# Optimization experiments

Hardware: AMD Instinct MI355X
Metric: run time of the kernel (lower is better)

Reference implementation:

```python
import jax, jax.numpy as jnp
import numpy as np


def _gen_grid(flow):
    # flow: [N, 2, H, W] -> grid [N, H, W, 2] in normalized [-1,1] coords
    N, _, H, W = flow.shape
    step_y = 2.0 / H
    step_x = 2.0 / W
    gy = jnp.arange(H, dtype=flow.dtype) * step_y + (-1.0 + 0.5 * step_y)
    gx = jnp.arange(W, dtype=flow.dtype) * step_x + (-1.0 + 0.5 * step_x)
    fp = jnp.transpose(flow, (0, 2, 3, 1))  # [N,H,W,2]
    fx = gx[None, None, :] + fp[..., 0]
    fy = gy[None, :, None] + fp[..., 1]
    fx = jnp.remainder(fx + 1.0, 2.0) - 1.0  # wrap x
    return jnp.stack([fx, fy], axis=-1)


def _grid_sample_bilinear(img, grid):
    # img: [N,C,H,W]; grid: [N,H,W,2] normalized, align_corners=False, zero padding
    N, C, H, W = img.shape
    ihwc = jnp.transpose(img, (0, 2, 3, 1))  # [N,H,W,C]
    x = (grid[..., 0] + 1.0) * (W * 0.5) - 0.5
    y = (grid[..., 1] + 1.0) * (H * 0.5) - 0.5
    x0 = jnp.floor(x)
    y0 = jnp.floor(y)
    tx = x - x0
    ty = y - y0
    x0i = x0.astype(jnp.int32)
    y0i = y0.astype(jnp.int32)
    n = jnp.arange(N)[:, None, None]

    def gather(yi, xi):
        valid = (xi >= 0) & (xi < W) & (yi >= 0) & (yi < H)
        v = ihwc[n, jnp.clip(yi, 0, H - 1), jnp.clip(xi, 0, W - 1)]  # [N,H,W,C]
        return v * valid[..., None].astype(img.dtype)

    out = (gather(y0i, x0i) * ((1 - tx) * (1 - ty))[..., None]
           + gather(y0i, x0i + 1) * (tx * (1 - ty))[..., None]
           + gather(y0i + 1, x0i) * ((1 - tx) * ty)[..., None]
           + gather(y0i + 1, x0i + 1) * (tx * ty)[..., None])
    return jnp.transpose(out, (0, 3, 1, 2))  # [N,C,H,W]


def _compose(flow_prev, img_prev, flow_curr, img_curr):
    grid = _gen_grid(flow_curr)
    return (flow_curr + _grid_sample_bilinear(flow_prev, grid),
            img_curr + _grid_sample_bilinear(img_prev, grid))


def setup_inputs() -> dict:
    key = jax.random.key(0)
    k1, k2 = jax.random.split(key)
    B, L, C, H, W = 4, 32, 32, 128, 128
    flows = jax.random.normal(k1, (B, L, 2, H, W), dtype=jnp.float32) * 0.05
    images = jax.random.normal(k2, (B, L, C, H, W), dtype=jnp.float32)
    return {"flows": flows, "images": images}


def reference(flows, images):
    B, L, _, H, W = flows.shape
    C = images.shape[2]
    cf, ci = flows, images
    step = 1
    while step < L:  # static log2(L) iterations
        Lp = L - step
        pf = cf[:, :-step].reshape(B * Lp, 2, H, W)
        pi = ci[:, :-step].reshape(B * Lp, C, H, W)
        qf = cf[:, step:].reshape(B * Lp, 2, H, W)
        qi = ci[:, step:].reshape(B * Lp, C, H, W)
        nf, ni = _compose(pf, pi, qf, qi)
        cf = jnp.concatenate([cf[:, :step], nf.reshape(B, Lp, 2, H, W)], axis=1)
        ci = jnp.concatenate([ci[:, :step], ni.reshape(B, Lp, C, H, W)], axis=1)
        step *= 2
    return ci
```

## Files before the change

kernel.cpp:

```cpp
#include <hip/hip_runtime.h>


constexpr int B_ = 4, L_ = 32, C_ = 32, H_ = 128, W_ = 128;
constexpr int HW = H_ * W_;
constexpr size_t SLICE_I = (size_t)C_ * HW;
constexpr size_t SLICE_F = (size_t)2  * HW;

typedef unsigned short ush;

__device__ __forceinline__ float b2f(ush u) {
    union { unsigned int i; float f; } v; v.i = ((unsigned int)u) << 16; return v.f;
}
__device__ __forceinline__ ush f2b(float f) {
    union { float f; unsigned int i; } v; v.f = f;
    unsigned int r = v.i + 0x7FFFu + ((v.i >> 16) & 1u);
    return (ush)(r >> 16);
}

__device__ __forceinline__ int swz8(int bid, int chunk) {
    return (bid & 7) * chunk + (bid >> 3);
}

__global__ __launch_bounds__(256)
void prepass_img(const float* __restrict__ src, ush* __restrict__ P,
                 ush* __restrict__ S, float* __restrict__ outN)
{
    constexpr int NB = 32 * 512;
    const int bid = swz8(blockIdx.x, NB / 8);
    const int wc = bid & 3, h = (bid >> 2) & 127, l = bid >> 9;
    __shared__ float lds[32 * 33];
    const int t = threadIdx.x;
    {
        const int c = t >> 3, wq = t & 7;
        const size_t off = (size_t)l * SLICE_I + (size_t)c * HW + h * W_ + wc * 32 + wq * 4;
        const float4 v = *(const float4*)(src + off);
        if (l == 0)
            *(float4*)(outN + off) = v;
        float* s = &lds[c * 33 + wq * 4];
        s[0] = v.x; s[1] = v.y; s[2] = v.z; s[3] = v.w;
    }
    __syncthreads();
    {
        const int pix = t >> 3, cc = t & 7;
        ushort4 o;
        o.x = f2b(lds[(cc * 4 + 0) * 33 + pix]);
        o.y = f2b(lds[(cc * 4 + 1) * 33 + pix]);
        o.z = f2b(lds[(cc * 4 + 2) * 33 + pix]);
        o.w = f2b(lds[(cc * 4 + 3) * 33 + pix]);
        const size_t poff = ((size_t)l * HW + h * W_ + wc * 32 + pix) * C_ + cc * 4;
        if (l == 0) *(ushort4*)(S + poff) = o;
        else        *(ushort4*)(P + poff) = o;
    }
}

__global__ __launch_bounds__(256)
void prepass_flow(const float* __restrict__ src, float* __restrict__ F0,
                  float* __restrict__ SF)
{
    constexpr int NB = 32 * HW / 256;
    const int i = swz8(blockIdx.x, NB / 8) * 256 + threadIdx.x;
    const int l = i >> 14;
    const int p = i & (HW - 1);
    const float f0 = src[(size_t)l * SLICE_F + p];
    const float f1 = src[(size_t)l * SLICE_F + HW + p];
    float* dst = (l == 0) ? SF : F0;
    *(float2*)(dst + (size_t)l * SLICE_F + (size_t)p * 2) = make_float2(f0, f1);
}

template<int STEP>
__global__ __launch_bounds__(256)
void compose(const float* __restrict__ Fcur, const ush* __restrict__ Icur,
             float* __restrict__ Fpong, ush* __restrict__ Ipong,
             ush* __restrict__ S, float* __restrict__ SF,
             float* __restrict__ outN)
{
#pragma clang fp contract(off)
    constexpr int NB = (32 - STEP) * 512;
    const int bid = swz8(blockIdx.x, NB / 8);
    const int wc = bid & 3, h = (bid >> 2) & 127, l = STEP + (bid >> 9);
    const int t = threadIdx.x, pix = t >> 3, cc = t & 7;
    const int w = wc * 32 + pix;
    const int p = h * W_ + w;
    const size_t sI = (size_t)l * SLICE_I;
    const size_t sF = (size_t)l * SLICE_F;

    const float2 fc = *(const float2*)(Fcur + sF + (size_t)p * 2);

    const float step_x = 2.0f / (float)W_;
    const float step_y = 2.0f / (float)H_;
    const float gx = (float)w * step_x + (-1.0f + 0.5f * step_x);
    const float gy = (float)h * step_y + (-1.0f + 0.5f * step_y);
    float fx = gx + fc.x;
    const float fy = gy + fc.y;
    {
        const float tt = fx + 1.0f;
        float r = fmodf(tt, 2.0f);
        if (r < 0.0f) r += 2.0f;
        fx = r - 1.0f;
    }
    const float x = (fx + 1.0f) * ((float)W_ * 0.5f) - 0.5f;
    const float y = (fy + 1.0f) * ((float)H_ * 0.5f) - 0.5f;
    const float x0f = floorf(x), y0f = floorf(y);
    const float tx = x - x0f, ty = y - y0f;
    const int x0 = (int)x0f, y0 = (int)y0f, x1 = x0 + 1, y1 = y0 + 1;
    const float w00 = (1.0f - tx) * (1.0f - ty);
    const float w10 = tx * (1.0f - ty);
    const float w01 = (1.0f - tx) * ty;
    const float w11 = tx * ty;
    const bool vx0 = (x0 >= 0) & (x0 < W_), vx1 = (x1 >= 0) & (x1 < W_);
    const bool vy0 = (y0 >= 0) & (y0 < H_), vy1 = (y1 >= 0) & (y1 < H_);
    const bool v00 = vy0 & vx0, v10 = vy0 & vx1, v01 = vy1 & vx0, v11 = vy1 & vx1;
    const int xc0 = x0 < 0 ? 0 : (x0 >= W_ ? W_ - 1 : x0);
    const int xc1 = x1 < 0 ? 0 : (x1 >= W_ ? W_ - 1 : x1);
    const int yc0 = y0 < 0 ? 0 : (y0 >= H_ ? H_ - 1 : y0);
    const int yc1 = y1 < 0 ? 0 : (y1 >= H_ ? H_ - 1 : y1);
    const int q00 = yc0 * W_ + xc0, q10 = yc0 * W_ + xc1;
    const int q01 = yc1 * W_ + xc0, q11 = yc1 * W_ + xc1;

    const int prev = l - STEP;
    const ush*   pI = (prev < STEP) ? (S  + (size_t)prev * SLICE_I)
                                    : (Icur + (size_t)prev * SLICE_I);
    const float* pF = (prev < STEP) ? (SF + (size_t)prev * SLICE_F)
                                    : (Fcur + (size_t)prev * SLICE_F);

    const ushort4 G00 = *(const ushort4*)(pI + (size_t)q00 * C_ + cc * 4);
    const ushort4 G10 = *(const ushort4*)(pI + (size_t)q10 * C_ + cc * 4);
    const ushort4 G01 = *(const ushort4*)(pI + (size_t)q01 * C_ + cc * 4);
    const ushort4 G11 = *(const ushort4*)(pI + (size_t)q11 * C_ + cc * 4);
    float4 g00 = make_float4(b2f(G00.x), b2f(G00.y), b2f(G00.z), b2f(G00.w));
    float4 g10 = make_float4(b2f(G10.x), b2f(G10.y), b2f(G10.z), b2f(G10.w));
    float4 g01 = make_float4(b2f(G01.x), b2f(G01.y), b2f(G01.z), b2f(G01.w));
    float4 g11 = make_float4(b2f(G11.x), b2f(G11.y), b2f(G11.z), b2f(G11.w));
    g00.x = v00 ? g00.x : 0.0f; g00.y = v00 ? g00.y : 0.0f;
    g00.z = v00 ? g00.z : 0.0f; g00.w = v00 ? g00.w : 0.0f;
    g10.x = v10 ? g10.x : 0.0f; g10.y = v10 ? g10.y : 0.0f;
    g10.z = v10 ? g10.z : 0.0f; g10.w = v10 ? g10.w : 0.0f;
    g01.x = v01 ? g01.x : 0.0f; g01.y = v01 ? g01.y : 0.0f;
    g01.z = v01 ? g01.z : 0.0f; g01.w = v01 ? g01.w : 0.0f;
    g11.x = v11 ? g11.x : 0.0f; g11.y = v11 ? g11.y : 0.0f;
    g11.z = v11 ? g11.z : 0.0f; g11.w = v11 ? g11.w : 0.0f;

    float4 samp;
    samp.x = ((g00.x * w00 + g10.x * w10) + g01.x * w01) + g11.x * w11;
    samp.y = ((g00.y * w00 + g10.y * w10) + g01.y * w01) + g11.y * w11;
    samp.z = ((g00.z * w00 + g10.z * w10) + g01.z * w01) + g11.z * w11;
    samp.w = ((g00.w * w00 + g10.w * w10) + g01.w * w01) + g11.w * w11;

    const ushort4 CU = *(const ushort4*)(Icur + sI + (size_t)p * C_ + cc * 4);
    float4 o;
    o.x = b2f(CU.x) + samp.x; o.y = b2f(CU.y) + samp.y;
    o.z = b2f(CU.z) + samp.z; o.w = b2f(CU.w) + samp.w;

    float2 fo;
    const bool doFlow = (cc == 0) && (STEP < 16);
    if (doFlow) {
        float2 A00 = *(const float2*)(pF + (size_t)q00 * 2);
        float2 A10 = *(const float2*)(pF + (size_t)q10 * 2);
        float2 A01 = *(const float2*)(pF + (size_t)q01 * 2);
        float2 A11 = *(const float2*)(pF + (size_t)q11 * 2);
        A00.x = v00 ? A00.x : 0.0f; A00.y = v00 ? A00.y : 0.0f;
        A10.x = v10 ? A10.x : 0.0f; A10.y = v10 ? A10.y : 0.0f;
        A01.x = v01 ? A01.x : 0.0f; A01.y = v01 ? A01.y : 0.0f;
        A11.x = v11 ? A11.x : 0.0f; A11.y = v11 ? A11.y : 0.0f;
        const float sx = ((A00.x * w00 + A10.x * w10) + A01.x * w01) + A11.x * w11;
        const float sy = ((A00.y * w00 + A10.y * w10) + A01.y * w01) + A11.y * w11;
        fo = make_float2(fc.x + sx, fc.y + sy);
    }

    __shared__ float lds[32 * 33];
    const bool fin = (STEP == 16) || (l < 2 * STEP);
    if (fin) {
        lds[(cc * 4 + 0) * 33 + pix] = o.x;
        lds[(cc * 4 + 1) * 33 + pix] = o.y;
        lds[(cc * 4 + 2) * 33 + pix] = o.z;
        lds[(cc * 4 + 3) * 33 + pix] = o.w;
        if constexpr (STEP < 16) {
            ushort4 ob = make_ushort4(f2b(o.x), f2b(o.y), f2b(o.z), f2b(o.w));
            *(ushort4*)(S + sI + (size_t)p * C_ + cc * 4) = ob;
            if (doFlow)
                *(float2*)(SF + sF + (size_t)p * 2) = fo;
        }
        __syncthreads();
        const int c = t >> 3, wq = t & 7;
        float4 ov;
        ov.x = lds[c * 33 + wq * 4 + 0];
        ov.y = lds[c * 33 + wq * 4 + 1];
        ov.z = lds[c * 33 + wq * 4 + 2];
        ov.w = lds[c * 33 + wq * 4 + 3];
        *(float4*)(outN + sI + (size_t)c * HW + h * W_ + wc * 32 + wq * 4) = ov;
    } else {
        ushort4 ob = make_ushort4(f2b(o.x), f2b(o.y), f2b(o.z), f2b(o.w));
        *(ushort4*)(Ipong + sI + (size_t)p * C_ + cc * 4) = ob;
        if (doFlow)
            *(float2*)(Fpong + sF + (size_t)p * 2) = fo;
    }
}

extern "C" void kernel_launch(void* const* d_in, const int* in_sizes, int n_in,
                              void* d_out, int out_size, void* d_ws, size_t ws_size,
                              hipStream_t stream)
{
    const float* inF = (const float*)d_in[0];
    const float* inI = (const float*)d_in[1];
    float* outI = (float*)d_out;

    char* ws = (char*)d_ws;
    ush*   P  = (ush*)  (ws);
    ush*   Q  = (ush*)  (ws + (size_t)(32 << 20));
    ush*   S  = (ush*)  (ws + (size_t)(64 << 20));
    float* F0 = (float*)(ws + (size_t)(80 << 20));
    float* F1 = (float*)(ws + (size_t)(84 << 20));
    float* SF = (float*)(ws + (size_t)(88 << 20));

    for (int b = 0; b < B_; ++b) {
        const float* bF = inF + (size_t)b * L_ * SLICE_F;
        const float* bI = inI + (size_t)b * L_ * SLICE_I;
        float* bO = outI + (size_t)b * L_ * SLICE_I;

        prepass_img <<<32 * 512, 256, 0, stream>>>(bI, P, S, bO);
        prepass_flow<<<32 * HW / 256, 256, 0, stream>>>(bF, F0, SF);

        compose<1> <<<31 * 512, 256, 0, stream>>>(F0, P, F1, Q, S, SF, bO);
        compose<2> <<<30 * 512, 256, 0, stream>>>(F1, Q, F0, P, S, SF, bO);
        compose<4> <<<28 * 512, 256, 0, stream>>>(F0, P, F1, Q, S, SF, bO);
        compose<8> <<<24 * 512, 256, 0, stream>>>(F1, Q, F0, P, S, SF, bO);
        compose<16><<<16 * 512, 256, 0, stream>>>(F0, P, F1, Q, S, SF, bO);
    }
}
```

Measured before the change: 876.2 us.

## Widen per-thread work to 8 channels and two rows per compose thread

Each compose thread now handles 8 bf16 channels via 16-byte loads/stores and processes two vertically adjacent pixels, cutting the grid by four. The prepass also covers 64 pixels per block with 8-channel packed stores. Validity masks are folded into the bilinear weights. This targets memory-instruction count and per-thread index overhead, at the cost of higher register pressure, fewer blocks, and extra barriers in the final-output path.

```diff
diff --git a/kernel.cpp b/kernel.cpp
--- a/kernel.cpp
+++ b/kernel.cpp
@@ -7,85 +7,36 @@
 constexpr size_t SLICE_F = (size_t)2  * HW;
 
 typedef unsigned short ush;
-
-__device__ __forceinline__ float b2f(ush u) {
-    union { unsigned int i; float f; } v; v.i = ((unsigned int)u) << 16; return v.f;
-}
-__device__ __forceinline__ ush f2b(float f) {
-    union { float f; unsigned int i; } v; v.f = f;
-    unsigned int r = v.i + 0x7FFFu + ((v.i >> 16) & 1u);
-    return (ush)(r >> 16);
+typedef unsigned int uint;
+
+__device__ __forceinline__ float uasf(uint u){ union{uint i;float f;}v; v.i=u; return v.f; }
+__device__ __forceinline__ uint fasu(float f){ union{float f;uint i;}v; v.f=f; return v.i; }
+__device__ __forceinline__ uint f2b_u(float f){ uint i=fasu(f); return (i + 0x7FFFu + ((i>>16)&1u))>>16; }
+
+__device__ __forceinline__ void unpack8(const uint4 u, float* f){
+    f[0]=uasf(u.x<<16); f[1]=uasf(u.x&0xFFFF0000u);
+    f[2]=uasf(u.y<<16); f[3]=uasf(u.y&0xFFFF0000u);
+    f[4]=uasf(u.z<<16); f[5]=uasf(u.z&0xFFFF0000u);
+    f[6]=uasf(u.w<<16); f[7]=uasf(u.w&0xFFFF0000u);
+}
+__device__ __forceinline__ uint4 pack8(const float* f){
+    uint4 u;
+    u.x = f2b_u(f[0]) | (f2b_u(f[1])<<16);
+    u.y = f2b_u(f[2]) | (f2b_u(f[3])<<16);
+    u.z = f2b_u(f[4]) | (f2b_u(f[5])<<16);
+    u.w = f2b_u(f[6]) | (f2b_u(f[7])<<16);
+    return u;
 }
 
 __device__ __forceinline__ int swz8(int bid, int chunk) {
     return (bid & 7) * chunk + (bid >> 3);
 }
 
-__global__ __launch_bounds__(256)
-void prepass_img(const float* __restrict__ src, ush* __restrict__ P,
-                 ush* __restrict__ S, float* __restrict__ outN)
-{
-    constexpr int NB = 32 * 512;
-    const int bid = swz8(blockIdx.x, NB / 8);
-    const int wc = bid & 3, h = (bid >> 2) & 127, l = bid >> 9;
-    __shared__ float lds[32 * 33];
-    const int t = threadIdx.x;
-    {
-        const int c = t >> 3, wq = t & 7;
-        const size_t off = (size_t)l * SLICE_I + (size_t)c * HW + h * W_ + wc * 32 + wq * 4;
-        const float4 v = *(const float4*)(src + off);
-        if (l == 0)
-            *(float4*)(outN + off) = v;
-        float* s = &lds[c * 33 + wq * 4];
-        s[0] = v.x; s[1] = v.y; s[2] = v.z; s[3] = v.w;
-    }
-    __syncthreads();
-    {
-        const int pix = t >> 3, cc = t & 7;
-        ushort4 o;
-        o.x = f2b(lds[(cc * 4 + 0) * 33 + pix]);
-        o.y = f2b(lds[(cc * 4 + 1) * 33 + pix]);
-        o.z = f2b(lds[(cc * 4 + 2) * 33 + pix]);
-        o.w = f2b(lds[(cc * 4 + 3) * 33 + pix]);
-        const size_t poff = ((size_t)l * HW + h * W_ + wc * 32 + pix) * C_ + cc * 4;
-        if (l == 0) *(ushort4*)(S + poff) = o;
-        else        *(ushort4*)(P + poff) = o;
-    }
-}
-
-__global__ __launch_bounds__(256)
-void prepass_flow(const float* __restrict__ src, float* __restrict__ F0,
-                  float* __restrict__ SF)
-{
-    constexpr int NB = 32 * HW / 256;
-    const int i = swz8(blockIdx.x, NB / 8) * 256 + threadIdx.x;
-    const int l = i >> 14;
-    const int p = i & (HW - 1);
-    const float f0 = src[(size_t)l * SLICE_F + p];
-    const float f1 = src[(size_t)l * SLICE_F + HW + p];
-    float* dst = (l == 0) ? SF : F0;
-    *(float2*)(dst + (size_t)l * SLICE_F + (size_t)p * 2) = make_float2(f0, f1);
-}
-
-template<int STEP>
-__global__ __launch_bounds__(256)
-void compose(const float* __restrict__ Fcur, const ush* __restrict__ Icur,
-             float* __restrict__ Fpong, ush* __restrict__ Ipong,
-             ush* __restrict__ S, float* __restrict__ SF,
-             float* __restrict__ outN)
+struct Samp { float wm00, wm10, wm01, wm11; int q00, q10, q01, q11; };
+
+__device__ __forceinline__ Samp mk(const float2 fc, const int w, const int h)
 {
 #pragma clang fp contract(off)
-    constexpr int NB = (32 - STEP) * 512;
-    const int bid = swz8(blockIdx.x, NB / 8);
-    const int wc = bid & 3, h = (bid >> 2) & 127, l = STEP + (bid >> 9);
-    const int t = threadIdx.x, pix = t >> 3, cc = t & 7;
-    const int w = wc * 32 + pix;
-    const int p = h * W_ + w;
-    const size_t sI = (size_t)l * SLICE_I;
-    const size_t sF = (size_t)l * SLICE_F;
-
-    const float2 fc = *(const float2*)(Fcur + sF + (size_t)p * 2);
-
     const float step_x = 2.0f / (float)W_;
     const float step_y = 2.0f / (float)H_;
     const float gx = (float)w * step_x + (-1.0f + 0.5f * step_x);
@@ -109,13 +60,98 @@
     const float w11 = tx * ty;
     const bool vx0 = (x0 >= 0) & (x0 < W_), vx1 = (x1 >= 0) & (x1 < W_);
     const bool vy0 = (y0 >= 0) & (y0 < H_), vy1 = (y1 >= 0) & (y1 < H_);
-    const bool v00 = vy0 & vx0, v10 = vy0 & vx1, v01 = vy1 & vx0, v11 = vy1 & vx1;
     const int xc0 = x0 < 0 ? 0 : (x0 >= W_ ? W_ - 1 : x0);
     const int xc1 = x1 < 0 ? 0 : (x1 >= W_ ? W_ - 1 : x1);
     const int yc0 = y0 < 0 ? 0 : (y0 >= H_ ? H_ - 1 : y0);
     const int yc1 = y1 < 0 ? 0 : (y1 >= H_ ? H_ - 1 : y1);
-    const int q00 = yc0 * W_ + xc0, q10 = yc0 * W_ + xc1;
-    const int q01 = yc1 * W_ + xc0, q11 = yc1 * W_ + xc1;
+    Samp s;
+    s.wm00 = (vy0 & vx0) ? w00 : 0.0f;
+    s.wm10 = (vy0 & vx1) ? w10 : 0.0f;
+    s.wm01 = (vy1 & vx0) ? w01 : 0.0f;
+    s.wm11 = (vy1 & vx1) ? w11 : 0.0f;
+    s.q00 = yc0 * W_ + xc0; s.q10 = yc0 * W_ + xc1;
+    s.q01 = yc1 * W_ + xc0; s.q11 = yc1 * W_ + xc1;
+    return s;
+}
+
+__device__ __forceinline__ float2 flowSamp(const float* __restrict__ pF,
+                                           const Samp s, const float2 fc)
+{
+#pragma clang fp contract(off)
+    const float2 a = *(const float2*)(pF + (size_t)s.q00 * 2);
+    const float2 b = *(const float2*)(pF + (size_t)s.q10 * 2);
+    const float2 c = *(const float2*)(pF + (size_t)s.q01 * 2);
+    const float2 d = *(const float2*)(pF + (size_t)s.q11 * 2);
+    const float sx = ((a.x * s.wm00 + b.x * s.wm10) + c.x * s.wm01) + d.x * s.wm11;
+    const float sy = ((a.y * s.wm00 + b.y * s.wm10) + c.y * s.wm01) + d.y * s.wm11;
+    return make_float2(fc.x + sx, fc.y + sy);
+}
+
+__global__ __launch_bounds__(256)
+void prepass_img(const float* __restrict__ src, ush* __restrict__ P,
+                 ush* __restrict__ S, float* __restrict__ outN)
+{
+    constexpr int NB = 32 * 256;
+    const int bid = swz8(blockIdx.x, NB / 8);
+    const int wc2 = bid & 1, h = (bid >> 1) & 127, l = bid >> 8;
+    __shared__ float lds[32][66];
+    const int t = threadIdx.x;
+    {
+        const int c = t >> 3, wq = t & 7;
+        const size_t base = (size_t)l * SLICE_I + (size_t)c * HW + h * W_ + wc2 * 64 + wq * 4;
+        const float4 v0 = *(const float4*)(src + base);
+        const float4 v1 = *(const float4*)(src + base + 32);
+        if (l == 0) {
+            *(float4*)(outN + base) = v0;
+            *(float4*)(outN + base + 32) = v1;
+        }
+        lds[c][wq*4+0] = v0.x; lds[c][wq*4+1] = v0.y;
+        lds[c][wq*4+2] = v0.z; lds[c][wq*4+3] = v0.w;
+        lds[c][wq*4+32] = v1.x; lds[c][wq*4+33] = v1.y;
+        lds[c][wq*4+34] = v1.z; lds[c][wq*4+35] = v1.w;
+    }
+    __syncthreads();
+    {
+        const int pg = t >> 2, lane4 = t & 3;
+        float f[8];
+        #pragma unroll
+        for (int j = 0; j < 8; ++j) f[j] = lds[lane4*8+j][pg];
+        ush* dst = (l == 0) ? S : P;
+        *(uint4*)(dst + ((size_t)l * HW + h * W_ + wc2 * 64 + pg) * C_ + lane4 * 8) = pack8(f);
+    }
+}
+
+__global__ __launch_bounds__(256)
+void prepass_flow(const float* __restrict__ src, float* __restrict__ F0,
+                  float* __restrict__ SF)
+{
+    constexpr int NB = 32 * HW / 256;
+    const int i = swz8(blockIdx.x, NB / 8) * 256 + threadIdx.x;
+    const int l = i >> 14;
+    const int p = i & (HW - 1);
+    const float f0 = src[(size_t)l * SLICE_F + p];
+    const float f1 = src[(size_t)l * SLICE_F + HW + p];
+    float* dst = (l == 0) ? SF : F0;
+    *(float2*)(dst + (size_t)l * SLICE_F + (size_t)p * 2) = make_float2(f0, f1);
+}
+
+template<int STEP>
+__global__ __launch_bounds__(256)
+void compose(const float* __restrict__ Fcur, const ush* __restrict__ Icur,
+             float* __restrict__ Fpong, ush* __restrict__ Ipong,
+             ush* __restrict__ S, float* __restrict__ SF,
+             float* __restrict__ outN)
+{
+#pragma clang fp contract(off)
+    constexpr int NB = (32 - STEP) * 128;
+    const int bid = swz8(blockIdx.x, NB / 8);
+    const int wc2 = bid & 1, h2 = (bid >> 1) & 63, l = STEP + (bid >> 7);
+    const int t = threadIdx.x, lane4 = t & 3, pg = t >> 2;
+    const int w = wc2 * 64 + pg;
+    const int hA = 2 * h2, hB = hA + 1;
+    const int pA = hA * W_ + w, pB = pA + W_;
+    const size_t sI = (size_t)l * SLICE_I;
+    const size_t sF = (size_t)l * SLICE_F;
 
     const int prev = l - STEP;
     const ush*   pI = (prev < STEP) ? (S  + (size_t)prev * SLICE_I)
@@ -123,76 +159,97 @@
     const float* pF = (prev < STEP) ? (SF + (size_t)prev * SLICE_F)
                                     : (Fcur + (size_t)prev * SLICE_F);
 
-    const ushort4 G00 = *(const ushort4*)(pI + (size_t)q00 * C_ + cc * 4);
-    const ushort4 G10 = *(const ushort4*)(pI + (size_t)q10 * C_ + cc * 4);
-    const ushort4 G01 = *(const ushort4*)(pI + (size_t)q01 * C_ + cc * 4);
-    const ushort4 G11 = *(const ushort4*)(pI + (size_t)q11 * C_ + cc * 4);
-    float4 g00 = make_float4(b2f(G00.x), b2f(G00.y), b2f(G00.z), b2f(G00.w));
-    float4 g10 = make_float4(b2f(G10.x), b2f(G10.y), b2f(G10.z), b2f(G10.w));
-    float4 g01 = make_float4(b2f(G01.x), b2f(G01.y), b2f(G01.z), b2f(G01.w));
-    float4 g11 = make_float4(b2f(G11.x), b2f(G11.y), b2f(G11.z), b2f(G11.w));
-    g00.x = v00 ? g00.x : 0.0f; g00.y = v00 ? g00.y : 0.0f;
-    g00.z = v00 ? g00.z : 0.0f; g00.w = v00 ? g00.w : 0.0f;
-    g10.x = v10 ? g10.x : 0.0f; g10.y = v10 ? g10.y : 0.0f;
-    g10.z = v10 ? g10.z : 0.0f; g10.w = v10 ? g10.w : 0.0f;
-    g01.x = v01 ? g01.x : 0.0f; g01.y = v01 ? g01.y : 0.0f;
-    g01.z = v01 ? g01.z : 0.0f; g01.w = v01 ? g01.w : 0.0f;
-    g11.x = v11 ? g11.x : 0.0f; g11.y = v11 ? g11.y : 0.0f;
-    g11.z = v11 ? g11.z : 0.0f; g11.w = v11 ? g11.w : 0.0f;
-
-    float4 samp;
-    samp.x = ((g00.x * w00 + g10.x * w10) + g01.x * w01) + g11.x * w11;
-    samp.y = ((g00.y * w00 + g10.y * w10) + g01.y * w01) + g11.y * w11;
-    samp.z = ((g00.z * w00 + g10.z * w10) + g01.z * w01) + g11.z * w11;
-    samp.w = ((g00.w * w00 + g10.w * w10) + g01.w * w01) + g11.w * w11;
-
-    const ushort4 CU = *(const ushort4*)(Icur + sI + (size_t)p * C_ + cc * 4);
-    float4 o;
-    o.x = b2f(CU.x) + samp.x; o.y = b2f(CU.y) + samp.y;
-    o.z = b2f(CU.z) + samp.z; o.w = b2f(CU.w) + samp.w;
-
-    float2 fo;
-    const bool doFlow = (cc == 0) && (STEP < 16);
+    const float2 fcA = *(const float2*)(Fcur + sF + (size_t)pA * 2);
+    const float2 fcB = *(const float2*)(Fcur + sF + (size_t)pB * 2);
+    const Samp sa = mk(fcA, w, hA);
+    const Samp sb = mk(fcB, w, hB);
+
+    const uint4 A00 = *(const uint4*)(pI + (size_t)sa.q00 * C_ + lane4 * 8);
+    const uint4 A10 = *(const uint4*)(pI + (size_t)sa.q10 * C_ + lane4 * 8);
+    const uint4 A01 = *(const uint4*)(pI + (size_t)sa.q01 * C_ + lane4 * 8);
+    const uint4 A11 = *(const uint4*)(pI + (size_t)sa.q11 * C_ + lane4 * 8);
+    const uint4 B00 = *(const uint4*)(pI + (size_t)sb.q00 * C_ + lane4 * 8);
+    const uint4 B10 = *(const uint4*)(pI + (size_t)sb.q10 * C_ + lane4 * 8);
+    const uint4 B01 = *(const uint4*)(pI + (size_t)sb.q01 * C_ + lane4 * 8);
+    const uint4 B11 = *(const uint4*)(pI + (size_t)sb.q11 * C_ + lane4 * 8);
+    const uint4 CA  = *(const uint4*)(Icur + sI + (size_t)pA * C_ + lane4 * 8);
+    const uint4 CB  = *(const uint4*)(Icur + sI + (size_t)pB * C_ + lane4 * 8);
+
+    float oA[8], oB[8];
+    {
+        float g0[8], g1[8], g2[8], g3[8], cu[8];
+        unpack8(A00, g0); unpack8(A10, g1); unpack8(A01, g2); unpack8(A11, g3);
+        unpack8(CA, cu);
+        #pragma unroll
+        for (int j = 0; j < 8; ++j) {
+            const float s_ = ((g0[j]*sa.wm00 + g1[j]*sa.wm10) + g2[j]*sa.wm01) + g3[j]*sa.wm11;
+            oA[j] = cu[j] + s_;
+        }
+        unpack8(B00, g0); unpack8(B10, g1); unpack8(B01, g2); unpack8(B11, g3);
+        unpack8(CB, cu);
+        #pragma unroll
+        for (int j = 0; j < 8; ++j) {
+            const float s_ = ((g0[j]*sb.wm00 + g1[j]*sb.wm10) + g2[j]*sb.wm01) + g3[j]*sb.wm11;
+            oB[j] = cu[j] + s_;
+        }
+    }
+
+    float2 foA, foB;
+    const bool doFlow = (lane4 == 0) && (STEP < 16);
     if (doFlow) {
-        float2 A00 = *(const float2*)(pF + (size_t)q00 * 2);
-        float2 A10 = *(const float2*)(pF + (size_t)q10 * 2);
-        float2 A01 = *(const float2*)(pF + (size_t)q01 * 2);
-        float2 A11 = *(const float2*)(pF + (size_t)q11 * 2);
-        A00.x = v00 ? A00.x : 0.0f; A00.y = v00 ? A00.y : 0.0f;
-        A10.x = v10 ? A10.x : 0.0f; A10.y = v10 ? A10.y : 0.0f;
-        A01.x = v01 ? A01.x : 0.0f; A01.y = v01 ? A01.y : 0.0f;
-        A11.x = v11 ? A11.x : 0.0f; A11.y = v11 ? A11.y : 0.0f;
-        const float sx = ((A00.x * w00 + A10.x * w10) + A01.x * w01) + A11.x * w11;
-        const float sy = ((A00.y * w00 + A10.y * w10) + A01.y * w01) + A11.y * w11;
-        fo = make_float2(fc.x + sx, fc.y + sy);
-    }
-
-    __shared__ float lds[32 * 33];
+        foA = flowSamp(pF, sa, fcA);
+        foB = flowSamp(pF, sb, fcB);
+    }
+
+    __shared__ float lds[32][66];
     const bool fin = (STEP == 16) || (l < 2 * STEP);
     if (fin) {
-        lds[(cc * 4 + 0) * 33 + pix] = o.x;
-        lds[(cc * 4 + 1) * 33 + pix] = o.y;
-        lds[(cc * 4 + 2) * 33 + pix] = o.z;
-        lds[(cc * 4 + 3) * 33 + pix] = o.w;
+        #pragma unroll
+        for (int j = 0; j < 8; ++j) lds[lane4*8+j][pg] = oA[j];
+        __syncthreads();
+        {
+            const int c = t >> 3, wq = t & 7;
+            float v[8];
+            #pragma unroll
+            for (int j2 = 0; j2 < 4; ++j2) {
+                const float2 e = *(const float2*)&lds[c][wq*8 + 2*j2];
+                v[2*j2] = e.x; v[2*j2+1] = e.y;
+            }
+            float* dst = outN + sI + (size_t)c * HW + hA * W_ + wc2 * 64 + wq * 8;
+            *(float4*)dst       = make_float4(v[0], v[1], v[2], v[3]);
+            *(float4*)(dst + 4) = make_float4(v[4], v[5], v[6], v[7]);
+        }
+        __syncthreads();
+        #pragma unroll
+        for (int j = 0; j < 8; ++j) lds[lane4*8+j][pg] = oB[j];
+        __syncthreads();
+        {
+            const int c = t >> 3, wq = t & 7;
+            float v[8];
+            #pragma unroll
+            for (int j2 = 0; j2 < 4; ++j2) {
+                const float2 e = *(const float2*)&lds[c][wq*8 + 2*j2];
+                v[2*j2] = e.x; v[2*j2+1] = e.y;
+            }
+            float* dst = outN + sI + (size_t)c * HW + hB * W_ + wc2 * 64 + wq * 8;
+            *(float4*)dst       = make_float4(v[0], v[1], v[2], v[3]);
+            *(float4*)(dst + 4) = make_float4(v[4], v[5], v[6], v[7]);
+        }
         if constexpr (STEP < 16) {
-            ushort4 ob = make_ushort4(f2b(o.x), f2b(o.y), f2b(o.z), f2b(o.w));
-            *(ushort4*)(S + sI + (size_t)p * C_ + cc * 4) = ob;
-            if (doFlow)
-                *(float2*)(SF + sF + (size_t)p * 2) = fo;
-        }
-        __syncthreads();
-        const int c = t >> 3, wq = t & 7;
-        float4 ov;
-        ov.x = lds[c * 33 + wq * 4 + 0];
-        ov.y = lds[c * 33 + wq * 4 + 1];
-        ov.z = lds[c * 33 + wq * 4 + 2];
-        ov.w = lds[c * 33 + wq * 4 + 3];
-        *(float4*)(outN + sI + (size_t)c * HW + h * W_ + wc * 32 + wq * 4) = ov;
+            *(uint4*)(S + sI + (size_t)pA * C_ + lane4 * 8) = pack8(oA);
+            *(uint4*)(S + sI + (size_t)pB * C_ + lane4 * 8) = pack8(oB);
+            if (doFlow) {
+                *(float2*)(SF + sF + (size_t)pA * 2) = foA;
+                *(float2*)(SF + sF + (size_t)pB * 2) = foB;
+            }
+        }
     } else {
-        ushort4 ob = make_ushort4(f2b(o.x), f2b(o.y), f2b(o.z), f2b(o.w));
-        *(ushort4*)(Ipong + sI + (size_t)p * C_ + cc * 4) = ob;
-        if (doFlow)
-            *(float2*)(Fpong + sF + (size_t)p * 2) = fo;
+        *(uint4*)(Ipong + sI + (size_t)pA * C_ + lane4 * 8) = pack8(oA);
+        *(uint4*)(Ipong + sI + (size_t)pB * C_ + lane4 * 8) = pack8(oB);
+        if (doFlow) {
+            *(float2*)(Fpong + sF + (size_t)pA * 2) = foA;
+            *(float2*)(Fpong + sF + (size_t)pB * 2) = foB;
+        }
     }
 }
 
@@ -217,13 +274,13 @@
         const float* bI = inI + (size_t)b * L_ * SLICE_I;
         float* bO = outI + (size_t)b * L_ * SLICE_I;
 
-        prepass_img <<<32 * 512, 256, 0, stream>>>(bI, P, S, bO);
+        prepass_img <<<32 * 256, 256, 0, stream>>>(bI, P, S, bO);
         prepass_flow<<<32 * HW / 256, 256, 0, stream>>>(bF, F0, SF);
 
-        compose<1> <<<31 * 512, 256, 0, stream>>>(F0, P, F1, Q, S, SF, bO);
-        compose<2> <<<30 * 512, 256, 0, stream>>>(F1, Q, F0, P, S, SF, bO);
-        compose<4> <<<28 * 512, 256, 0, stream>>>(F0, P, F1, Q, S, SF, bO);
-        compose<8> <<<24 * 512, 256, 0, stream>>>(F1, Q, F0, P, S, SF, bO);
-        compose<16><<<16 * 512, 256, 0, stream>>>(F0, P, F1, Q, S, SF, bO);
-    }
-}
+        compose<1> <<<31 * 128, 256, 0, stream>>>(F0, P, F1, Q, S, SF, bO);
+        compose<2> <<<30 * 128, 256, 0, stream>>>(F1, Q, F0, P, S, SF, bO);
+        compose<4> <<<28 * 128, 256, 0, stream>>>(F0, P, F1, Q, S, SF, bO);
+        compose<8> <<<24 * 128, 256, 0, stream>>>(F1, Q, F0, P, S, SF, bO);
+        compose<16><<<16 * 128, 256, 0, stream>>>(F0, P, F1, Q, S, SF, bO);
+    }
+}
```

Result: faster. 847.7 us (-3.2%).
